# Kernel tuning notes

Hardware: AMD Instinct MI355X
Metric: run time of the kernel (lower is better)

Reference implementation:

```python
import jax, jax.numpy as jnp
import numpy as np
import math

GROUPS = 32
EPS = 1e-5
NUM_HEADS = 8


def group_norm(x, gamma, beta):
    # x: [B, C, H, W]; normalize within each of GROUPS channel groups over (C/G, H, W)
    B, C, H, W = x.shape
    xg = x.reshape(B, GROUPS, C // GROUPS, H, W)
    mean = jnp.mean(xg, axis=(2, 3, 4), keepdims=True)
    var = jnp.var(xg, axis=(2, 3, 4), keepdims=True)
    xn = ((xg - mean) * jax.lax.rsqrt(var + EPS)).reshape(B, C, H, W)
    return xn * gamma[None, :, None, None] + beta[None, :, None, None]


def setup_inputs() -> dict:
    key = jax.random.key(0)
    ks = jax.random.split(key, 10)
    C = 512
    B, H, W = 2, 64, 64
    s = 1.0 / math.sqrt(C)
    return {
        "x": jax.random.normal(ks[0], (B, C, H, W), jnp.float32),
        "gamma": jnp.ones((C,), jnp.float32),
        "beta": jnp.zeros((C,), jnp.float32),
        "Wq": jax.random.normal(ks[1], (C, C), jnp.float32) * s,
        "bq": jax.random.normal(ks[2], (C,), jnp.float32) * 0.01,
        "Wk": jax.random.normal(ks[3], (C, C), jnp.float32) * s,
        "bk": jax.random.normal(ks[4], (C,), jnp.float32) * 0.01,
        "Wv": jax.random.normal(ks[5], (C, C), jnp.float32) * s,
        "bv": jax.random.normal(ks[6], (C,), jnp.float32) * 0.01,
        "Wo": jax.random.normal(ks[7], (C, C), jnp.float32) * s,
        "bo": jax.random.normal(ks[8], (C,), jnp.float32) * 0.01,
    }


def reference(x, gamma, beta, Wq, bq, Wk, bk, Wv, bv, Wo, bo):
    B, C, H, W = x.shape
    N = H * W
    hd = C // NUM_HEADS
    h = group_norm(x, gamma, beta)
    h = h.reshape(B, C, N).transpose(0, 2, 1)  # [B, N, C]
    # torch nn.Linear: y = x @ W.T + b
    q = (h @ Wq.T + bq).reshape(B, N, NUM_HEADS, hd)
    k = (h @ Wk.T + bk).reshape(B, N, NUM_HEADS, hd)
    v = (h @ Wv.T + bv).reshape(B, N, NUM_HEADS, hd)
    scale = 1.0 / math.sqrt(hd)
    attn = jnp.einsum('bihd,bjhd->bijh', q, k) * scale  # [B, N, N, heads]
    attn = jax.nn.softmax(attn, axis=2)
    o = jnp.einsum('bijh,bjhd->bihd', attn, v).reshape(B, N, C)
    o = o @ Wo.T + bo
    o = o.transpose(0, 2, 1).reshape(B, C, H, W)
    return x + o
```

## Files before the change

kernel.cpp:

```cpp
#include <hip/hip_runtime.h>
#include <cstdint>
#include <cstddef>

typedef __bf16 bf16x8 __attribute__((ext_vector_type(8)));
typedef float f32x4 __attribute__((ext_vector_type(4)));
typedef float f32x16 __attribute__((ext_vector_type(16)));
typedef unsigned short ushort8 __attribute__((ext_vector_type(8)));
typedef unsigned u32x2 __attribute__((ext_vector_type(2)));
typedef float f4 __attribute__((ext_vector_type(4)));

__device__ __forceinline__ unsigned short f2bf(float f) {
    __bf16 b = (__bf16)f;
    return *(unsigned short*)&b;
}
__device__ __forceinline__ unsigned pk2bf(float a, float b) {
    __bf16 x = (__bf16)a, y = (__bf16)b;
    unsigned short ux = *(unsigned short*)&x, uy = *(unsigned short*)&y;
    return (unsigned)ux | ((unsigned)uy << 16);
}
__device__ __forceinline__ float bf2f(unsigned short u) {
    union { unsigned u; float f; } v; v.u = ((unsigned)u) << 16; return v.f;
}

#if __has_builtin(__builtin_amdgcn_exp2f)
#define EXP2(x) __builtin_amdgcn_exp2f(x)
#else
#define EXP2(x) exp2f(x)
#endif

__device__ __forceinline__ void pl32swap(unsigned& x, unsigned& y) {
#if __has_builtin(__builtin_amdgcn_permlane32_swap)
    auto r = __builtin_amdgcn_permlane32_swap(x, y, false, false);
    x = r[0]; y = r[1];
#else
    unsigned xs = (unsigned)__shfl_xor((int)x, 32, 64);
    unsigned ys = (unsigned)__shfl_xor((int)y, 32, 64);
    bool lo = ((threadIdx.x & 63) < 32);
    unsigned nx = lo ? x : ys;
    unsigned ny = lo ? xs : y;
    x = nx; y = ny;
#endif
}

#define GLL(g, l) __builtin_amdgcn_global_load_lds( \
    (__attribute__((address_space(1))) void*)(g), \
    (__attribute__((address_space(3))) void*)(l), 16, 0, 0)

#define CS 0.18033688011112042f
#define SPLITS 4

__global__ __launch_bounds__(256) void convert_w(
    const float* __restrict__ wq, const float* __restrict__ wk,
    const float* __restrict__ wv, const float* __restrict__ wo,
    unsigned short* __restrict__ out)
{
    int i = blockIdx.x * 256 + threadIdx.x;
    const float* src = (i < 262144) ? wq : (i < 524288) ? wk : (i < 786432) ? wv : wo;
    out[i] = f2bf(src[i & 262143]);
}

__global__ __launch_bounds__(256) void gn_stats(
    const float* __restrict__ x, float* __restrict__ part)
{
    const int q = blockIdx.x, bg = blockIdx.y;
    const f4* xv = (const f4*)(x + (size_t)bg * 65536 + q * 16384);
    float s = 0.f, sq = 0.f;
    for (int i = threadIdx.x; i < 4096; i += 256) {
        f4 v = xv[i];
        s  += v.x + v.y + v.z + v.w;
        sq += v.x * v.x + v.y * v.y + v.z * v.z + v.w * v.w;
    }
    #pragma unroll
    for (int off = 32; off > 0; off >>= 1) {
        s  += __shfl_xor(s, off, 64);
        sq += __shfl_xor(sq, off, 64);
    }
    __shared__ float red[8];
    const int w = threadIdx.x >> 6, lane = threadIdx.x & 63;
    if (lane == 0) { red[w] = s; red[4 + w] = sq; }
    __syncthreads();
    if (threadIdx.x == 0) {
        part[(bg * 4 + q) * 2]     = red[0] + red[1] + red[2] + red[3];
        part[(bg * 4 + q) * 2 + 1] = red[4] + red[5] + red[6] + red[7];
    }
}

__global__ __launch_bounds__(256) void gn_apply(
    const float* __restrict__ x, const float* __restrict__ gamma,
    const float* __restrict__ beta, const float* __restrict__ part,
    unsigned short* __restrict__ h)
{
    const int q = blockIdx.x, bg = blockIdx.y;
    const int b = bg >> 5, g = bg & 31;
    float s = 0.f, sq = 0.f;
    #pragma unroll
    for (int j = 0; j < 4; ++j) {
        s  += part[(bg * 4 + j) * 2];
        sq += part[(bg * 4 + j) * 2 + 1];
    }
    const float mean = s * (1.f / 65536.f);
    const float rstd = rsqrtf(sq * (1.f / 65536.f) - mean * mean + 1e-5f);

    float gm[16], bt[16];
    #pragma unroll
    for (int c = 0; c < 16; ++c) {
        gm[c] = gamma[g * 16 + c] * rstd;
        bt[c] = beta[g * 16 + c];
    }
    const float* xg = x + (size_t)bg * 65536;
    const int n0 = q * 1024 + threadIdx.x * 4;
    float val[16][4];
    #pragma unroll
    for (int c = 0; c < 16; ++c) {
        f4 v = *(const f4*)&xg[(size_t)c * 4096 + n0];
        val[c][0] = (v.x - mean) * gm[c] + bt[c];
        val[c][1] = (v.y - mean) * gm[c] + bt[c];
        val[c][2] = (v.z - mean) * gm[c] + bt[c];
        val[c][3] = (v.w - mean) * gm[c] + bt[c];
    }
    #pragma unroll
    for (int nn = 0; nn < 4; ++nn) {
        ushort8 v0, v1;
        #pragma unroll
        for (int c = 0; c < 8; ++c)  v0[c]     = f2bf(val[c][nn]);
        #pragma unroll
        for (int c = 8; c < 16; ++c) v1[c - 8] = f2bf(val[c][nn]);
        unsigned short* dst = h + ((size_t)(b * 4096 + n0 + nn)) * 512 + g * 16;
        *(ushort8*)dst = v0;
        *(ushort8*)(dst + 8) = v1;
    }
}

template <int MODE>
__global__ __launch_bounds__(256, 2) void gemm_bt(
    const unsigned short* __restrict__ A,
    const unsigned short* __restrict__ Bt,
    const float* __restrict__ bias0,
    const float* __restrict__ bias1,
    const float* __restrict__ bias2,
    const float* __restrict__ resid,
    void* __restrict__ outp,
    unsigned short* __restrict__ vtout,
    int M, int N, int K)
{
    __shared__ __attribute__((aligned(16))) unsigned short As[128 * 32];
    __shared__ __attribute__((aligned(16))) unsigned short Bs[128 * 32];
    const int t = threadIdx.x;
    const int w = t >> 6, lane = t & 63;
    const int l15 = lane & 15, l4 = lane >> 4;
    const int bm = blockIdx.y, bn = blockIdx.x;
    const int wm = (w >> 1) * 64, wn = (w & 1) * 64;

    f32x4 acc[4][4] = {};

    const int srow = t >> 2;
    const int sc8  = (t & 3) * 8;

    const unsigned short* gA0 = A  + (size_t)(bm * 128 + srow) * K + sc8;
    const unsigned short* gA1 = gA0 + (size_t)64 * K;
    const unsigned short* gB0 = Bt + (size_t)(bn * 128 + srow) * K + sc8;
    const unsigned short* gB1 = gB0 + (size_t)64 * K;
    unsigned short* lA0 = &As[w * 512];
    unsigned short* lA1 = &As[2048 + w * 512];
    unsigned short* lB0 = &Bs[w * 512];
    unsigned short* lB1 = &Bs[2048 + w * 512];

    for (int k0 = 0; k0 < K; k0 += 32) {
        __syncthreads();
        GLL(gA0 + k0, lA0);
        GLL(gA1 + k0, lA1);
        GLL(gB0 + k0, lB0);
        GLL(gB1 + k0, lB1);
        __syncthreads();

        bf16x8 af[4], bfr[4];
        #pragma unroll
        for (int mt = 0; mt < 4; ++mt)
            af[mt] = *(const bf16x8*)&As[(wm + mt * 16 + l15) * 32 + l4 * 8];
        #pragma unroll
        for (int nt = 0; nt < 4; ++nt)
            bfr[nt] = *(const bf16x8*)&Bs[(wn + nt * 16 + l15) * 32 + l4 * 8];
        #pragma unroll
        for (int mt = 0; mt < 4; ++mt)
            #pragma unroll
            for (int nt = 0; nt < 4; ++nt)
                acc[mt][nt] = __builtin_amdgcn_mfma_f32_16x16x32_bf16(
                    af[mt], bfr[nt], acc[mt][nt], 0, 0, 0);
    }

    if (MODE == 0) {
        unsigned short* outB = (unsigned short*)outp;
        #pragma unroll
        for (int nt = 0; nt < 4; ++nt) {
            int col = bn * 128 + wn + nt * 16 + l15;
            const float* bp = (col < 512) ? bias0 : (col < 1024) ? bias1 : bias2;
            float bv = bp[col & 511];
            if (col < 1024) {
                float sc = (col < 512) ? CS : 1.0f;
                #pragma unroll
                for (int mt = 0; mt < 4; ++mt)
                    #pragma unroll
                    for (int r = 0; r < 4; ++r) {
                        int row = bm * 128 + wm + mt * 16 + l4 * 4 + r;
                        outB[(size_t)row * 1024 + col] = f2bf((acc[mt][nt][r] + bv) * sc);
                    }
            } else {
                int hd = col - 1024;
                #pragma unroll
                for (int mt = 0; mt < 4; ++mt) {
                    int m = bm * 128 + wm + mt * 16 + l4 * 4;
                    int bb = m >> 12, n = m & 4095;
                    unsigned u0 = pk2bf(acc[mt][nt][0] + bv, acc[mt][nt][1] + bv);
                    unsigned u1 = pk2bf(acc[mt][nt][2] + bv, acc[mt][nt][3] + bv);
                    unsigned short* dst = vtout +
                        ((size_t)(bb * 8 + (hd >> 6)) * 64 + (hd & 63)) * 4096 + n;
                    *(u32x2*)dst = (u32x2){u0, u1};
                }
            }
        }
    } else {
        float* outF = (float*)outp;
        #pragma unroll
        for (int mt = 0; mt < 4; ++mt)
            #pragma unroll
            for (int nt = 0; nt < 4; ++nt)
                #pragma unroll
                for (int r = 0; r < 4; ++r) {
                    int c = bm * 128 + wm + mt * 16 + l4 * 4 + r;
                    int m = bn * 128 + wn + nt * 16 + l15;
                    int b = m >> 12, n = m & 4095;
                    size_t idx = ((size_t)(b * 512 + c)) * 4096 + n;
                    outF[idx] = acc[mt][nt][r] + bias0[c] + resid[idx];
                }
    }
}

__global__ __launch_bounds__(256, 2) void attn_kernel(
    const unsigned short* __restrict__ qkv, const unsigned short* __restrict__ vt,
    unsigned short* __restrict__ opart, float* __restrict__ lbuf)
{
    __shared__ __attribute__((aligned(16))) unsigned short Sh[2 * 64 * 72];
    unsigned short* KsB  = Sh;
    unsigned short* VtsB = Sh + 64 * 72;

    const int bh = blockIdx.y, b = bh >> 3, h = bh & 7;
    const int qbase = blockIdx.x * 256;
    const int s = blockIdx.z, ks0 = s * 1024;
    const int t = threadIdx.x, w = t >> 6, lane = t & 63;
    const int l31 = lane & 31, h5 = lane >> 5;

    const unsigned short* Qg = qkv + ((size_t)(b * 4096 + qbase + w * 64)) * 1024 + h * 64;
    const unsigned short* Kg = qkv + ((size_t)(b * 4096 + ks0)) * 1024 + 512 + h * 64;
    const unsigned short* Vg = vt + ((size_t)bh) * 64 * 4096 + ks0;

    bf16x8 qf[2][4];
    #pragma unroll
    for (int qt = 0; qt < 2; ++qt)
        #pragma unroll
        for (int kc = 0; kc < 4; ++kc)
            qf[qt][kc] = *(const bf16x8*)(Qg + (size_t)(qt * 32 + l31) * 1024 + kc * 16 + h5 * 8);

    f32x16 Oacc[2][2] = {};
    float li[2] = {0.f, 0.f};

    const int sr = t >> 2, sc = (t & 3) * 16;
    const unsigned short* gK = Kg + (size_t)sr * 1024 + sc;
    const unsigned short* gV = Vg + (size_t)sr * 4096 + sc;
    unsigned short* lK = KsB + sr * 72 + sc;
    unsigned short* lV = VtsB + sr * 72 + sc;

    ushort8 kr[2], vr[2];
    kr[0] = *(const ushort8*)(gK);
    kr[1] = *(const ushort8*)(gK + 8);
    vr[0] = *(const ushort8*)(gV);
    vr[1] = *(const ushort8*)(gV + 8);

    for (int kt = 0; kt < 16; ++kt) {
        __syncthreads();
        *(ushort8*)(lK)     = kr[0];
        *(ushort8*)(lK + 8) = kr[1];
        *(ushort8*)(lV)     = vr[0];
        *(ushort8*)(lV + 8) = vr[1];
        __syncthreads();
        if (kt < 15) {
            const unsigned short* nk = gK + (size_t)(kt + 1) * 64 * 1024;
            const unsigned short* nv = gV + (kt + 1) * 64;
            kr[0] = *(const ushort8*)(nk);
            kr[1] = *(const ushort8*)(nk + 8);
            vr[0] = *(const ushort8*)(nv);
            vr[1] = *(const ushort8*)(nv + 8);
        }

        f32x16 St[2][2] = {};
        #pragma unroll
        for (int ct = 0; ct < 2; ++ct)
            #pragma unroll
            for (int kc = 0; kc < 4; ++kc) {
                bf16x8 kf = *(const bf16x8*)(KsB + (ct * 32 + l31) * 72 + kc * 16 + h5 * 8);
                St[0][ct] = __builtin_amdgcn_mfma_f32_32x32x16_bf16(kf, qf[0][kc], St[0][ct], 0, 0, 0);
                St[1][ct] = __builtin_amdgcn_mfma_f32_32x32x16_bf16(kf, qf[1][kc], St[1][ct], 0, 0, 0);
            }

        union PU { unsigned u[4]; bf16x8 v; };
        PU pf[2][4];
        #pragma unroll
        for (int qt = 0; qt < 2; ++qt) {
            #pragma unroll
            for (int ct = 0; ct < 2; ++ct)
                #pragma unroll
                for (int r = 0; r < 16; ++r)
                    St[qt][ct][r] = EXP2(St[qt][ct][r]);
            float s0 = 0.f, s1 = 0.f;
            #pragma unroll
            for (int ct = 0; ct < 2; ++ct) {
                s0 += ((St[qt][ct][0] + St[qt][ct][1]) + (St[qt][ct][2] + St[qt][ct][3]))
                    + ((St[qt][ct][4] + St[qt][ct][5]) + (St[qt][ct][6] + St[qt][ct][7]));
                s1 += ((St[qt][ct][8] + St[qt][ct][9]) + (St[qt][ct][10] + St[qt][ct][11]))
                    + ((St[qt][ct][12] + St[qt][ct][13]) + (St[qt][ct][14] + St[qt][ct][15]));
            }
            li[qt] += s0 + s1;

            #pragma unroll
            for (int ct = 0; ct < 2; ++ct) {
                unsigned pk0 = pk2bf(St[qt][ct][0],  St[qt][ct][1]);
                unsigned pk1 = pk2bf(St[qt][ct][2],  St[qt][ct][3]);
                unsigned pk2 = pk2bf(St[qt][ct][4],  St[qt][ct][5]);
                unsigned pk3 = pk2bf(St[qt][ct][6],  St[qt][ct][7]);
                unsigned pk4 = pk2bf(St[qt][ct][8],  St[qt][ct][9]);
                unsigned pk5 = pk2bf(St[qt][ct][10], St[qt][ct][11]);
                unsigned pk6 = pk2bf(St[qt][ct][12], St[qt][ct][13]);
                unsigned pk7 = pk2bf(St[qt][ct][14], St[qt][ct][15]);
                pl32swap(pk0, pk2); pl32swap(pk1, pk3);
                pl32swap(pk4, pk6); pl32swap(pk5, pk7);
                pf[qt][ct * 2].u[0] = pk0; pf[qt][ct * 2].u[1] = pk1;
                pf[qt][ct * 2].u[2] = pk2; pf[qt][ct * 2].u[3] = pk3;
                pf[qt][ct * 2 + 1].u[0] = pk4; pf[qt][ct * 2 + 1].u[1] = pk5;
                pf[qt][ct * 2 + 1].u[2] = pk6; pf[qt][ct * 2 + 1].u[3] = pk7;
            }
        }

        #pragma unroll
        for (int kk = 0; kk < 4; ++kk)
            #pragma unroll
            for (int dt = 0; dt < 2; ++dt) {
                bf16x8 vf = *(const bf16x8*)(VtsB + (dt * 32 + l31) * 72 + kk * 16 + h5 * 8);
                Oacc[dt][0] = __builtin_amdgcn_mfma_f32_32x32x16_bf16(vf, pf[0][kk].v, Oacc[dt][0], 0, 0, 0);
                Oacc[dt][1] = __builtin_amdgcn_mfma_f32_32x32x16_bf16(vf, pf[1][kk].v, Oacc[dt][1], 0, 0, 0);
            }
    }

    #pragma unroll
    for (int qt = 0; qt < 2; ++qt) {
        float lf = li[qt] + __shfl_xor(li[qt], 32, 64);
        if (h5 == 0)
            lbuf[((size_t)s * 16 + bh) * 4096 + qbase + w * 64 + qt * 32 + l31] = lf;
    }

    __syncthreads();
    unsigned short* Eb = Sh + w * (32 * 72);
    #pragma unroll
    for (int qt = 0; qt < 2; ++qt) {
        #pragma unroll
        for (int dt = 0; dt < 2; ++dt)
            #pragma unroll
            for (int p = 0; p < 8; ++p) {
                int d = dt * 32 + 2 * (p & 1) + 8 * (p >> 1) + 4 * h5;
                unsigned u = pk2bf(Oacc[dt][qt][2 * p], Oacc[dt][qt][2 * p + 1]);
                *(unsigned*)&Eb[l31 * 72 + d] = u;
            }
        unsigned short* Og = opart +
            (((size_t)s * 16 + bh) * 4096 + qbase + w * 64 + qt * 32) * 64;
        #pragma unroll
        for (int i = 0; i < 4; ++i) {
            int c8 = h5 * 4 + i;
            ushort8 val = *(const ushort8*)&Eb[l31 * 72 + c8 * 8];
            *(ushort8*)(Og + (size_t)l31 * 64 + c8 * 8) = val;
        }
    }
}

__global__ __launch_bounds__(256) void combine_o(
    const unsigned short* __restrict__ opart, const float* __restrict__ lbuf,
    unsigned short* __restrict__ o)
{
    int gid = blockIdx.x * 256 + threadIdx.x;
    int row = gid >> 3, c8 = gid & 7;
    int bh = row >> 12, q = row & 4095;
    int b = bh >> 3, h = bh & 7;
    float l = 0.f;
    #pragma unroll
    for (int sp = 0; sp < SPLITS; ++sp)
        l += lbuf[(size_t)sp * 65536 + row];
    float inv = 1.f / l;
    float acc[8] = {};
    #pragma unroll
    for (int sp = 0; sp < SPLITS; ++sp) {
        ushort8 ov = *(const ushort8*)(opart +
            (size_t)sp * 65536 * 64 + (size_t)row * 64 + c8 * 8);
        #pragma unroll
        for (int i = 0; i < 8; ++i) acc[i] += bf2f(ov[i]);
    }
    ushort8 r;
    #pragma unroll
    for (int i = 0; i < 8; ++i) r[i] = f2bf(acc[i] * inv);
    *(ushort8*)(o + ((size_t)(b * 4096 + q)) * 512 + h * 64 + c8 * 8) = r;
}

extern "C" void kernel_launch(void* const* d_in, const int* in_sizes, int n_in,
                              void* d_out, int out_size, void* d_ws, size_t ws_size,
                              hipStream_t stream) {
    const float* x     = (const float*)d_in[0];
    const float* gamma = (const float*)d_in[1];
    const float* beta  = (const float*)d_in[2];
    const float* Wq    = (const float*)d_in[3];
    const float* bq    = (const float*)d_in[4];
    const float* Wk    = (const float*)d_in[5];
    const float* bk    = (const float*)d_in[6];
    const float* Wv    = (const float*)d_in[7];
    const float* bv    = (const float*)d_in[8];
    const float* Wo    = (const float*)d_in[9];
    const float* bo    = (const float*)d_in[10];
    float* out = (float*)d_out;

    char* ws = (char*)d_ws;
    const size_t MB = 1024 * 1024;
    unsigned short* wb     = (unsigned short*)(ws);
    float*          gnpart = (float*)(ws + 2 * MB);
    unsigned short* qkv    = (unsigned short*)(ws + 3 * MB);
    unsigned short* vtb    = (unsigned short*)(ws + 19 * MB);
    unsigned short* h      = (unsigned short*)(ws + 27 * MB);
    unsigned short* opart  = (unsigned short*)(ws + 27 * MB);
    float*          lbuf   = (float*)(ws + 59 * MB);
    unsigned short* obuf   = qkv;

    convert_w<<<dim3(4096), dim3(256), 0, stream>>>(Wq, Wk, Wv, Wo, wb);
    gn_stats<<<dim3(4, 64), dim3(256), 0, stream>>>(x, gnpart);
    gn_apply<<<dim3(4, 64), dim3(256), 0, stream>>>(x, gamma, beta, gnpart, h);

    gemm_bt<0><<<dim3(12, 64), dim3(256), 0, stream>>>(
        h, wb, bq, bk, bv, nullptr, qkv, vtb, 8192, 1536, 512);

    attn_kernel<<<dim3(16, 16, SPLITS), dim3(256), 0, stream>>>(qkv, vtb, opart, lbuf);
    combine_o<<<dim3(2048), dim3(256), 0, stream>>>(opart, lbuf, obuf);

    gemm_bt<1><<<dim3(64, 4), dim3(256), 0, stream>>>(
        wb + 786432, obuf, bo, nullptr, nullptr, x, out, nullptr, 512, 8192, 512);
}
```

Baseline: 230.6 us.

## Double-buffer K/V tiles with direct global-to-LDS loads in attention kernel

Replaces the register-staged K/V tile loads with direct global-to-LDS loads (GLL) into a double-buffered shared-memory layout, so the next tile streams in while the current one is computed and each iteration needs one barrier instead of two. The LDS layout becomes a fragment-ordered unpadded arrangement that matches the MFMA operand reads. The S computation is restructured per query tile to lower live accumulator registers, and launch bounds rise to 3 blocks per SM for higher occupancy. The risks are register spills under the tighter bound and possible LDS bank conflicts with the new layout.

```diff
diff --git a/kernel.cpp b/kernel.cpp
--- a/kernel.cpp
+++ b/kernel.cpp
@@ -235,13 +235,12 @@
     }
 }
 
-__global__ __launch_bounds__(256, 2) void attn_kernel(
+__global__ __launch_bounds__(256, 3) void attn_kernel(
     const unsigned short* __restrict__ qkv, const unsigned short* __restrict__ vt,
     unsigned short* __restrict__ opart, float* __restrict__ lbuf)
 {
-    __shared__ __attribute__((aligned(16))) unsigned short Sh[2 * 64 * 72];
-    unsigned short* KsB  = Sh;
-    unsigned short* VtsB = Sh + 64 * 72;
+    __shared__ __attribute__((aligned(16))) unsigned short Sh[16384];
+    char* ShB = (char*)Sh;
 
     const int bh = blockIdx.y, b = bh >> 3, h = bh & 7;
     const int qbase = blockIdx.x * 256;
@@ -263,73 +262,67 @@
     f32x16 Oacc[2][2] = {};
     float li[2] = {0.f, 0.f};
 
-    const int sr = t >> 2, sc = (t & 3) * 16;
-    const unsigned short* gK = Kg + (size_t)sr * 1024 + sc;
-    const unsigned short* gV = Vg + (size_t)sr * 4096 + sc;
-    unsigned short* lK = KsB + sr * 72 + sc;
-    unsigned short* lV = VtsB + sr * 72 + sc;
-
-    ushort8 kr[2], vr[2];
-    kr[0] = *(const ushort8*)(gK);
-    kr[1] = *(const ushort8*)(gK + 8);
-    vr[0] = *(const ushort8*)(gV);
-    vr[1] = *(const ushort8*)(gV + 8);
-
+    const unsigned short* gK0 = Kg + (size_t)lane * 1024 + w * 16;
+    const unsigned short* gK1 = gK0 + 8;
+    const unsigned short* gV0 = Vg + (size_t)lane * 4096 + w * 16;
+    const unsigned short* gV1 = gV0 + 8;
+    const int lk = w * 2048;
+    const int lv = 8192 + w * 2048;
+
+    const int rbase = h5 * 1024 + l31 * 16;
+
+    GLL(gK0, ShB + lk);
+    GLL(gK1, ShB + lk + 1024);
+    GLL(gV0, ShB + lv);
+    GLL(gV1, ShB + lv + 1024);
+    __syncthreads();
+
+    int cur = 0;
     for (int kt = 0; kt < 16; ++kt) {
-        __syncthreads();
-        *(ushort8*)(lK)     = kr[0];
-        *(ushort8*)(lK + 8) = kr[1];
-        *(ushort8*)(lV)     = vr[0];
-        *(ushort8*)(lV + 8) = vr[1];
-        __syncthreads();
         if (kt < 15) {
-            const unsigned short* nk = gK + (size_t)(kt + 1) * 64 * 1024;
-            const unsigned short* nv = gV + (kt + 1) * 64;
-            kr[0] = *(const ushort8*)(nk);
-            kr[1] = *(const ushort8*)(nk + 8);
-            vr[0] = *(const ushort8*)(nv);
-            vr[1] = *(const ushort8*)(nv + 8);
+            const size_t ko = (size_t)(kt + 1) * 65536;
+            const int    vo = (kt + 1) * 64;
+            char* nb = ShB + (cur ^ 1) * 16384;
+            GLL(gK0 + ko, nb + lk);
+            GLL(gK1 + ko, nb + lk + 1024);
+            GLL(gV0 + vo, nb + lv);
+            GLL(gV1 + vo, nb + lv + 1024);
         }
 
-        f32x16 St[2][2] = {};
-        #pragma unroll
-        for (int ct = 0; ct < 2; ++ct)
-            #pragma unroll
-            for (int kc = 0; kc < 4; ++kc) {
-                bf16x8 kf = *(const bf16x8*)(KsB + (ct * 32 + l31) * 72 + kc * 16 + h5 * 8);
-                St[0][ct] = __builtin_amdgcn_mfma_f32_32x32x16_bf16(kf, qf[0][kc], St[0][ct], 0, 0, 0);
-                St[1][ct] = __builtin_amdgcn_mfma_f32_32x32x16_bf16(kf, qf[1][kc], St[1][ct], 0, 0, 0);
-            }
+        const char* Kr = ShB + cur * 16384 + rbase;
+        const char* Vr = Kr + 8192;
 
         union PU { unsigned u[4]; bf16x8 v; };
         PU pf[2][4];
         #pragma unroll
         for (int qt = 0; qt < 2; ++qt) {
+            f32x16 St[2] = {};
             #pragma unroll
             for (int ct = 0; ct < 2; ++ct)
                 #pragma unroll
+                for (int kc = 0; kc < 4; ++kc) {
+                    bf16x8 kf = *(const bf16x8*)(Kr + kc * 2048 + ct * 512);
+                    St[ct] = __builtin_amdgcn_mfma_f32_32x32x16_bf16(
+                        kf, qf[qt][kc], St[ct], 0, 0, 0);
+                }
+            #pragma unroll
+            for (int ct = 0; ct < 2; ++ct) {
+                #pragma unroll
                 for (int r = 0; r < 16; ++r)
-                    St[qt][ct][r] = EXP2(St[qt][ct][r]);
-            float s0 = 0.f, s1 = 0.f;
-            #pragma unroll
-            for (int ct = 0; ct < 2; ++ct) {
-                s0 += ((St[qt][ct][0] + St[qt][ct][1]) + (St[qt][ct][2] + St[qt][ct][3]))
-                    + ((St[qt][ct][4] + St[qt][ct][5]) + (St[qt][ct][6] + St[qt][ct][7]));
-                s1 += ((St[qt][ct][8] + St[qt][ct][9]) + (St[qt][ct][10] + St[qt][ct][11]))
-                    + ((St[qt][ct][12] + St[qt][ct][13]) + (St[qt][ct][14] + St[qt][ct][15]));
-            }
-            li[qt] += s0 + s1;
-
-            #pragma unroll
-            for (int ct = 0; ct < 2; ++ct) {
-                unsigned pk0 = pk2bf(St[qt][ct][0],  St[qt][ct][1]);
-                unsigned pk1 = pk2bf(St[qt][ct][2],  St[qt][ct][3]);
-                unsigned pk2 = pk2bf(St[qt][ct][4],  St[qt][ct][5]);
-                unsigned pk3 = pk2bf(St[qt][ct][6],  St[qt][ct][7]);
-                unsigned pk4 = pk2bf(St[qt][ct][8],  St[qt][ct][9]);
-                unsigned pk5 = pk2bf(St[qt][ct][10], St[qt][ct][11]);
-                unsigned pk6 = pk2bf(St[qt][ct][12], St[qt][ct][13]);
-                unsigned pk7 = pk2bf(St[qt][ct][14], St[qt][ct][15]);
+                    St[ct][r] = EXP2(St[ct][r]);
+                li[qt] += ((St[ct][0] + St[ct][1]) + (St[ct][2] + St[ct][3]))
+                        + ((St[ct][4] + St[ct][5]) + (St[ct][6] + St[ct][7]))
+                        + ((St[ct][8] + St[ct][9]) + (St[ct][10] + St[ct][11]))
+                        + ((St[ct][12] + St[ct][13]) + (St[ct][14] + St[ct][15]));
+
+                unsigned pk0 = pk2bf(St[ct][0],  St[ct][1]);
+                unsigned pk1 = pk2bf(St[ct][2],  St[ct][3]);
+                unsigned pk2 = pk2bf(St[ct][4],  St[ct][5]);
+                unsigned pk3 = pk2bf(St[ct][6],  St[ct][7]);
+                unsigned pk4 = pk2bf(St[ct][8],  St[ct][9]);
+                unsigned pk5 = pk2bf(St[ct][10], St[ct][11]);
+                unsigned pk6 = pk2bf(St[ct][12], St[ct][13]);
+                unsigned pk7 = pk2bf(St[ct][14], St[ct][15]);
                 pl32swap(pk0, pk2); pl32swap(pk1, pk3);
                 pl32swap(pk4, pk6); pl32swap(pk5, pk7);
                 pf[qt][ct * 2].u[0] = pk0; pf[qt][ct * 2].u[1] = pk1;
@@ -343,10 +336,13 @@
         for (int kk = 0; kk < 4; ++kk)
             #pragma unroll
             for (int dt = 0; dt < 2; ++dt) {
-                bf16x8 vf = *(const bf16x8*)(VtsB + (dt * 32 + l31) * 72 + kk * 16 + h5 * 8);
+                bf16x8 vf = *(const bf16x8*)(Vr + kk * 2048 + dt * 512);
                 Oacc[dt][0] = __builtin_amdgcn_mfma_f32_32x32x16_bf16(vf, pf[0][kk].v, Oacc[dt][0], 0, 0, 0);
                 Oacc[dt][1] = __builtin_amdgcn_mfma_f32_32x32x16_bf16(vf, pf[1][kk].v, Oacc[dt][1], 0, 0, 0);
             }
+
+        __syncthreads();
+        cur ^= 1;
     }
 
     #pragma unroll
@@ -356,7 +352,6 @@
             lbuf[((size_t)s * 16 + bh) * 4096 + qbase + w * 64 + qt * 32 + l31] = lf;
     }
 
-    __syncthreads();
     unsigned short* Eb = Sh + w * (32 * 72);
     #pragma unroll
     for (int qt = 0; qt < 2; ++qt) {
```

Measured after the change: 293.2 us. +27.1%, slower.

## Double-buffer K/V tiles in attention, halve key splits, add MFMA priority hints

Applied to the files above, without the earlier changes.

The attention kernel now double-buffers the K and V^T shared-memory tiles, so the next tile is stored while the current one is consumed, with a single barrier per iteration instead of two. The key-dimension split count drops from 4 to 2, so each block walks 32 key tiles instead of 16; this means fewer partial outputs to combine but half as many blocks in the grid. s_setprio hints are placed around the MFMA sections, and the row-sum reduction is rewritten as packed two-wide float adds. Shared memory use grows to two buffers, and the reduced grid may hurt occupancy across the GPU's CUs.

```diff
diff --git a/kernel.cpp b/kernel.cpp
--- a/kernel.cpp
+++ b/kernel.cpp
@@ -3,6 +3,7 @@
 #include <cstddef>
 
 typedef __bf16 bf16x8 __attribute__((ext_vector_type(8)));
+typedef float f32x2 __attribute__((ext_vector_type(2)));
 typedef float f32x4 __attribute__((ext_vector_type(4)));
 typedef float f32x16 __attribute__((ext_vector_type(16)));
 typedef unsigned short ushort8 __attribute__((ext_vector_type(8)));
@@ -47,7 +48,7 @@
     (__attribute__((address_space(3))) void*)(l), 16, 0, 0)
 
 #define CS 0.18033688011112042f
-#define SPLITS 4
+#define SPLITS 2
 
 __global__ __launch_bounds__(256) void convert_w(
     const float* __restrict__ wq, const float* __restrict__ wk,
@@ -239,13 +240,11 @@
     const unsigned short* __restrict__ qkv, const unsigned short* __restrict__ vt,
     unsigned short* __restrict__ opart, float* __restrict__ lbuf)
 {
-    __shared__ __attribute__((aligned(16))) unsigned short Sh[2 * 64 * 72];
-    unsigned short* KsB  = Sh;
-    unsigned short* VtsB = Sh + 64 * 72;
+    __shared__ __attribute__((aligned(16))) unsigned short Sh[2 * 9216];
 
     const int bh = blockIdx.y, b = bh >> 3, h = bh & 7;
     const int qbase = blockIdx.x * 256;
-    const int s = blockIdx.z, ks0 = s * 1024;
+    const int s = blockIdx.z, ks0 = s * 2048;
     const int t = threadIdx.x, w = t >> 6, lane = t & 63;
     const int l31 = lane & 31, h5 = lane >> 5;
 
@@ -266,40 +265,58 @@
     const int sr = t >> 2, sc = (t & 3) * 16;
     const unsigned short* gK = Kg + (size_t)sr * 1024 + sc;
     const unsigned short* gV = Vg + (size_t)sr * 4096 + sc;
-    unsigned short* lK = KsB + sr * 72 + sc;
-    unsigned short* lV = VtsB + sr * 72 + sc;
+    const int soff = sr * 72 + sc;
 
     ushort8 kr[2], vr[2];
     kr[0] = *(const ushort8*)(gK);
     kr[1] = *(const ushort8*)(gK + 8);
     vr[0] = *(const ushort8*)(gV);
     vr[1] = *(const ushort8*)(gV + 8);
-
-    for (int kt = 0; kt < 16; ++kt) {
-        __syncthreads();
-        *(ushort8*)(lK)     = kr[0];
-        *(ushort8*)(lK + 8) = kr[1];
-        *(ushort8*)(lV)     = vr[0];
-        *(ushort8*)(lV + 8) = vr[1];
-        __syncthreads();
-        if (kt < 15) {
-            const unsigned short* nk = gK + (size_t)(kt + 1) * 64 * 1024;
-            const unsigned short* nv = gV + (kt + 1) * 64;
+    {
+        unsigned short* dK = &Sh[soff];
+        *(ushort8*)(dK)          = kr[0];
+        *(ushort8*)(dK + 8)      = kr[1];
+        *(ushort8*)(dK + 4608)     = vr[0];
+        *(ushort8*)(dK + 4608 + 8) = vr[1];
+    }
+    kr[0] = *(const ushort8*)(gK + 65536);
+    kr[1] = *(const ushort8*)(gK + 65536 + 8);
+    vr[0] = *(const ushort8*)(gV + 64);
+    vr[1] = *(const ushort8*)(gV + 64 + 8);
+    __syncthreads();
+
+    for (int kt = 0; kt < 32; ++kt) {
+        const int cur = kt & 1;
+        if (kt < 31) {
+            unsigned short* dK = &Sh[(cur ^ 1) * 9216 + soff];
+            *(ushort8*)(dK)          = kr[0];
+            *(ushort8*)(dK + 8)      = kr[1];
+            *(ushort8*)(dK + 4608)     = vr[0];
+            *(ushort8*)(dK + 4608 + 8) = vr[1];
+        }
+        if (kt < 30) {
+            const unsigned short* nk = gK + (size_t)(kt + 2) * 65536;
+            const unsigned short* nv = gV + (kt + 2) * 64;
             kr[0] = *(const ushort8*)(nk);
             kr[1] = *(const ushort8*)(nk + 8);
             vr[0] = *(const ushort8*)(nv);
             vr[1] = *(const ushort8*)(nv + 8);
         }
 
+        const unsigned short* Ks  = &Sh[cur * 9216];
+        const unsigned short* Vts = Ks + 4608;
+
         f32x16 St[2][2] = {};
+        __builtin_amdgcn_s_setprio(1);
         #pragma unroll
         for (int ct = 0; ct < 2; ++ct)
             #pragma unroll
             for (int kc = 0; kc < 4; ++kc) {
-                bf16x8 kf = *(const bf16x8*)(KsB + (ct * 32 + l31) * 72 + kc * 16 + h5 * 8);
+                bf16x8 kf = *(const bf16x8*)&Ks[(ct * 32 + l31) * 72 + kc * 16 + h5 * 8];
                 St[0][ct] = __builtin_amdgcn_mfma_f32_32x32x16_bf16(kf, qf[0][kc], St[0][ct], 0, 0, 0);
                 St[1][ct] = __builtin_amdgcn_mfma_f32_32x32x16_bf16(kf, qf[1][kc], St[1][ct], 0, 0, 0);
             }
+        __builtin_amdgcn_s_setprio(0);
 
         union PU { unsigned u[4]; bf16x8 v; };
         PU pf[2][4];
@@ -310,15 +327,16 @@
                 #pragma unroll
                 for (int r = 0; r < 16; ++r)
                     St[qt][ct][r] = EXP2(St[qt][ct][r]);
-            float s0 = 0.f, s1 = 0.f;
-            #pragma unroll
-            for (int ct = 0; ct < 2; ++ct) {
-                s0 += ((St[qt][ct][0] + St[qt][ct][1]) + (St[qt][ct][2] + St[qt][ct][3]))
-                    + ((St[qt][ct][4] + St[qt][ct][5]) + (St[qt][ct][6] + St[qt][ct][7]));
-                s1 += ((St[qt][ct][8] + St[qt][ct][9]) + (St[qt][ct][10] + St[qt][ct][11]))
-                    + ((St[qt][ct][12] + St[qt][ct][13]) + (St[qt][ct][14] + St[qt][ct][15]));
-            }
-            li[qt] += s0 + s1;
+
+            f32x2 ps = {0.f, 0.f};
+            #pragma unroll
+            for (int ct = 0; ct < 2; ++ct)
+                #pragma unroll
+                for (int r = 0; r < 16; r += 2) {
+                    f32x2 e = {St[qt][ct][r], St[qt][ct][r + 1]};
+                    ps += e;
+                }
+            li[qt] += ps[0] + ps[1];
 
             #pragma unroll
             for (int ct = 0; ct < 2; ++ct) {
@@ -339,14 +357,18 @@
             }
         }
 
+        __builtin_amdgcn_s_setprio(1);
         #pragma unroll
         for (int kk = 0; kk < 4; ++kk)
             #pragma unroll
             for (int dt = 0; dt < 2; ++dt) {
-                bf16x8 vf = *(const bf16x8*)(VtsB + (dt * 32 + l31) * 72 + kk * 16 + h5 * 8);
+                bf16x8 vf = *(const bf16x8*)&Vts[(dt * 32 + l31) * 72 + kk * 16 + h5 * 8];
                 Oacc[dt][0] = __builtin_amdgcn_mfma_f32_32x32x16_bf16(vf, pf[0][kk].v, Oacc[dt][0], 0, 0, 0);
                 Oacc[dt][1] = __builtin_amdgcn_mfma_f32_32x32x16_bf16(vf, pf[1][kk].v, Oacc[dt][1], 0, 0, 0);
             }
+        __builtin_amdgcn_s_setprio(0);
+
+        __syncthreads();
     }
 
     #pragma unroll
@@ -356,7 +378,6 @@
             lbuf[((size_t)s * 16 + bh) * 4096 + qbase + w * 64 + qt * 32 + l31] = lf;
     }
 
-    __syncthreads();
     unsigned short* Eb = Sh + w * (32 * 72);
     #pragma unroll
     for (int qt = 0; qt < 2; ++qt) {
```

Result: no change. 226.8 us (-1.6%).
